# Performance work log

Hardware: AMD Instinct MI355X
Metric: run time of the kernel (lower is better)

The kernel has to match this reference:

```python
import jax, jax.numpy as jnp
import numpy as np

B, S, HID = 2, 2048, 2048
H, HD, RD, LD = 16, 128, 64, 512
AD = HD + RD  # attn_dim = 192
SCALE = 1.0 / np.sqrt(AD)


def apply_rope(x):
    """x: [B, H, S, RD] -> RoPE-rotated, matching the torch RotaryEmbedding."""
    s = x.shape[2]
    inv_freq = 1.0 / (10000.0 ** (jnp.arange(0, RD, 2, dtype=jnp.float32) / RD))
    t = jnp.arange(s, dtype=x.dtype)
    freqs = t[:, None] * inv_freq[None, :]          # [S, RD//2]
    cos, sin = jnp.cos(freqs), jnp.sin(freqs)       # broadcast over B, H
    x1, x2 = x[..., : RD // 2], x[..., RD // 2 :]
    return jnp.concatenate([x1 * cos - x2 * sin, x2 * cos + x1 * sin], axis=-1)


def setup_inputs() -> dict:
    key = jax.random.key(0)
    ks = jax.random.split(key, 7)
    std = 0.02
    return {
        "x": jax.random.normal(ks[0], (B, S, HID), jnp.float32),
        # weights stored as [in, out] (transpose of torch Linear.weight)
        "wq": jax.random.normal(ks[1], (HID, H * HD), jnp.float32) * std,
        "wq_rope": jax.random.normal(ks[2], (HID, H * RD), jnp.float32) * std,
        "wkv_down": jax.random.normal(ks[3], (HID, LD), jnp.float32) * std,
        "wkv_up": jax.random.normal(ks[4], (LD, H * 2 * HD), jnp.float32) * std,
        "wk_rope": jax.random.normal(ks[5], (HID, RD), jnp.float32) * std,
        "wo": jax.random.normal(ks[6], (H * AD, HID), jnp.float32) * std,
    }


def reference(x, wq, wq_rope, wkv_down, wkv_up, wk_rope, wo):
    b, s, _ = x.shape
    # query paths
    q_nope = (x @ wq).reshape(b, s, H, HD).transpose(0, 2, 1, 3)        # [B,H,S,HD]
    q_rope = (x @ wq_rope).reshape(b, s, H, RD).transpose(0, 2, 1, 3)   # [B,H,S,RD]
    q_rope = apply_rope(q_rope)
    q = jnp.concatenate([q_nope, q_rope], axis=-1)                      # [B,H,S,AD]
    # low-rank KV latent upcast
    kv_latent = x @ wkv_down                                            # [B,S,LD]
    kv = (kv_latent @ wkv_up).reshape(b, s, H, 2 * HD).transpose(0, 2, 1, 3)
    k_nope, v = kv[..., :HD], kv[..., HD:]                              # [B,H,S,HD]
    # shared rope key, broadcast over heads
    k_rope = jnp.broadcast_to((x @ wk_rope)[:, None], (b, H, s, RD))
    k_rope = apply_rope(k_rope)
    k = jnp.concatenate([k_nope, k_rope], axis=-1)                      # [B,H,S,AD]
    # zero-pad V to attn_dim
    v_pad = jnp.pad(v, ((0, 0), (0, 0), (0, 0), (0, RD)))
    # attention (causal)
    scores = jnp.einsum("bhqd,bhkd->bhqk", q, k) * SCALE
    causal = jnp.tril(jnp.ones((s, s), bool))
    scores = jnp.where(causal, scores, jnp.finfo(scores.dtype).min)
    probs = jax.nn.softmax(scores, axis=-1)
    attn = jnp.einsum("bhqk,bhkd->bhqd", probs, v_pad)                  # [B,H,S,AD]
    attn = attn.transpose(0, 2, 1, 3).reshape(b, s, H * AD)
    return attn @ wo
```

## Files before the change

kernel.cpp:

```cpp
#include <hip/hip_runtime.h>
#include <math.h>

#define HB 2
#define HS 2048
#define HHID 2048
#define HH 16
#define HHD 128
#define HRD 64
#define HLD 512
#define HAD 192
#define HM (HB*HS)

static __device__ __constant__ float C1_SCALE_LOG2E = 0.1041175465f;

typedef unsigned short US;
typedef __attribute__((ext_vector_type(8))) short s8v;
typedef __attribute__((ext_vector_type(4))) float f4v;
typedef __attribute__((ext_vector_type(16))) float f16v;

#if __has_builtin(__builtin_amdgcn_exp2f)
#define EXP2F __builtin_amdgcn_exp2f
#else
#define EXP2F exp2f
#endif

__device__ __forceinline__ US f2b(float f){
  union { float f; unsigned u; } v; v.f = f;
  unsigned r = v.u + 0x7fffu + ((v.u >> 16) & 1u);
  return (US)(r >> 16);
}
__device__ __forceinline__ float b2f(US u){
  union { unsigned u; float f; } v; v.u = ((unsigned)u) << 16; return v.f;
}
__device__ __forceinline__ f4v mfma16(s8v a, s8v b, f4v c){
  return __builtin_amdgcn_mfma_f32_16x16x32_bf16(a, b, c, 0, 0, 0);
}
__device__ __forceinline__ f16v mfma32(s8v a, s8v b, f16v c){
  return __builtin_amdgcn_mfma_f32_32x32x16_bf16(a, b, c, 0, 0, 0);
}
__device__ __forceinline__ void gload_lds16(const void* g, void* l){
  __builtin_amdgcn_global_load_lds((const __attribute__((address_space(1))) void*)g,
                                   (__attribute__((address_space(3))) void*)l, 16, 0, 0);
}

__global__ __launch_bounds__(256) void k_cast(const float* __restrict__ in, US* __restrict__ out, int n){
  int i = (blockIdx.x * 256 + threadIdx.x) * 4;
  if (i >= n) return;
  float4 v = *(const float4*)(in + i);
  union { US q[4]; unsigned u[2]; } p;
  p.q[0] = f2b(v.x); p.q[1] = f2b(v.y); p.q[2] = f2b(v.z); p.q[3] = f2b(v.w);
  *(uint2*)(out + i) = make_uint2(p.u[0], p.u[1]);
}

__global__ __launch_bounds__(256) void k_rope_tab(float2* __restrict__ tab){
  int idx = blockIdx.x * 256 + threadIdx.x;
  int s = idx >> 5, i = idx & 31;
  float invf = expf(-9.210340371976184f * (float)i / 32.f);
  float fr = (float)s * invf;
  tab[idx] = make_float2(cosf(fr), sinf(fr));
}

template<int WOMAP>
__global__ __launch_bounds__(256) void k_transpose_cast(const float* __restrict__ W, US* __restrict__ Wt, int K, int N){
  __shared__ float t[32][33];
  int n0 = blockIdx.x * 32, k0 = blockIdx.y * 32;
  int tx = threadIdx.x, ty = threadIdx.y;
  #pragma unroll
  for (int r = 0; r < 32; r += 8){
    int k = k0 + ty + r;
    int sk = WOMAP ? ((k >> 7) * 192 + (k & 127)) : k;
    t[ty + r][tx] = W[(size_t)sk * N + n0 + tx];
  }
  __syncthreads();
  #pragma unroll
  for (int r = 0; r < 32; r += 8){
    Wt[(size_t)(n0 + ty + r) * K + k0 + tx] = f2b(t[tx][ty + r]);
  }
}

__global__ __launch_bounds__(256) void k_transpose_v(const US* __restrict__ v, US* __restrict__ vT){
  __shared__ US t[32][33];
  int bh = blockIdx.z;
  int s0 = blockIdx.x * 32, d0 = blockIdx.y * 32;
  const US* src = v + (size_t)bh * HS * HHD;
  US* dst = vT + (size_t)bh * HHD * HS;
  int tx = threadIdx.x, ty = threadIdx.y;
  #pragma unroll
  for (int r = 0; r < 32; r += 8)
    t[ty + r][tx] = src[(size_t)(s0 + ty + r) * HHD + d0 + tx];
  __syncthreads();
  #pragma unroll
  for (int r = 0; r < 32; r += 8)
    dst[(size_t)(d0 + ty + r) * HS + s0 + tx] = t[tx][ty + r];
}

template<int EPI>
__global__ __launch_bounds__(256, 2) void k_gemm2(
    const US* __restrict__ A, const US* __restrict__ Bt,
    void* __restrict__ out0, void* __restrict__ out1, void* __restrict__ out2,
    int Kdim, int Ndim)
{
  __shared__ US As[2][128 * 64];
  __shared__ US Bs[2][128 * 64];
  const int tid = threadIdx.x;
  const int lane = tid & 63, w = tid >> 6;
  const int r15 = lane & 15, kh = lane >> 4;
  const int gx = gridDim.x;
  const int flat = blockIdx.y * gx + blockIdx.x;
  const int cpx = (gx * gridDim.y) >> 3;
  const int swz = (flat & 7) * cpx + (flat >> 3);
  const int m0 = (swz / gx) * 128, n0 = (swz % gx) * 128;
  const int wm = (w >> 1) * 64, wn = (w & 1) * 64;
  const int rsw = (r15 & 7) << 4;
  f4v acc[4][4] = {};

  auto STAGE = [&](int k0, int bb){
    #pragma unroll
    for (int j = 0; j < 4; ++j){
      int c = j * 256 + tid;
      int row = c >> 3, colD = (c & 7) * 16;
      gload_lds16((const char*)A + ((size_t)(m0 + row) * Kdim + k0) * 2 + (colD ^ ((row & 7) << 4)),
                  (char*)As[bb] + c * 16);
    }
    #pragma unroll
    for (int j = 0; j < 4; ++j){
      int c = j * 256 + tid;
      int row = c >> 3, colD = (c & 7) * 16;
      gload_lds16((const char*)Bt + ((size_t)(n0 + row) * Kdim + k0) * 2 + (colD ^ ((row & 7) << 4)),
                  (char*)Bs[bb] + c * 16);
    }
  };

  const int nk = Kdim >> 6;
  STAGE(0, 0);
  for (int t = 0; t < nk; ++t){
    if (t + 1 < nk){
      STAGE((t + 1) * 64, (t + 1) & 1);
      asm volatile("s_waitcnt vmcnt(8)" ::: "memory");
    } else {
      asm volatile("s_waitcnt vmcnt(0)" ::: "memory");
    }
    __builtin_amdgcn_s_barrier();
    __builtin_amdgcn_sched_barrier(0);
    const char* AB = (const char*)As[t & 1];
    const char* BB = (const char*)Bs[t & 1];
    #pragma unroll
    for (int ks = 0; ks < 2; ++ks){
      s8v af[4];
      #pragma unroll
      for (int mi = 0; mi < 4; ++mi)
        af[mi] = *(const s8v*)(AB + (wm + mi * 16 + r15) * 128 + ((ks * 64 + kh * 16) ^ rsw));
      #pragma unroll
      for (int ni = 0; ni < 4; ++ni){
        s8v bf = *(const s8v*)(BB + (wn + ni * 16 + r15) * 128 + ((ks * 64 + kh * 16) ^ rsw));
        #pragma unroll
        for (int mi = 0; mi < 4; ++mi)
          acc[mi][ni] = mfma16(af[mi], bf, acc[mi][ni]);
      }
    }
    __builtin_amdgcn_s_barrier();
  }

  #pragma unroll
  for (int mi = 0; mi < 4; ++mi){
    #pragma unroll
    for (int ni = 0; ni < 4; ++ni){
      #pragma unroll
      for (int j = 0; j < 4; ++j){
        float v = acc[mi][ni][j];
        int m = m0 + wm + mi * 16 + kh * 4 + j;
        int n = n0 + wn + ni * 16 + r15;
        if (EPI == 3){
          int b = m >> 11, s = m & 2047;
          int h = n >> 8, r = n & 255;
          if (r < 128)
            ((US*)out0)[((size_t)(b * HH + h) * HS + s) * HAD + r] = f2b(v);
          else
            ((US*)out1)[((size_t)(b * HH + h) * HS + s) * HHD + (r - 128)] = f2b(v);
        } else if (EPI == 4){
          ((float*)out0)[(size_t)m * HHID + n] = v;
        } else {
          int b = m >> 11, s = m & 2047;
          if (n < 2048){
            int h = n >> 7, d = n & 127;
            ((US*)out0)[((size_t)(b * HH + h) * HS + s) * HAD + d] = f2b(v);
          } else if (n < 3072){
            int dd2 = n - 2048;
            int h = dd2 >> 6, dd = dd2 & 63;
            float partner = acc[mi][ni ^ 2][j];
            float2 cs = ((const float2*)out1)[s * 32 + (dd & 31)];
            float o = (dd < 32) ? (v * cs.x - partner * cs.y) : (v * cs.x + partner * cs.y);
            ((US*)out0)[((size_t)(b * HH + h) * HS + s) * HAD + HHD + dd] = f2b(o);
          } else {
            ((US*)out2)[(size_t)m * HLD + (n - 3072)] = f2b(v);
          }
        }
      }
    }
  }
}

__global__ __launch_bounds__(256) void k_krope2(const US* __restrict__ A, const US* __restrict__ Bt,
                                                US* __restrict__ kbuf, const float2* __restrict__ tab)
{
  __shared__ US As[2][128 * 32];
  __shared__ US Bs[2][64 * 32];
  const int tid = threadIdx.x, lane = tid & 63, w = tid >> 6;
  const int r15 = lane & 15, kh = lane >> 4;
  const int m0 = blockIdx.x * 128;
  const int wm = w * 32;
  f4v acc[2][4] = {};

  auto STAGE = [&](int k0, int bb){
    #pragma unroll
    for (int j = 0; j < 2; ++j){
      int c = (w * 2 + j) * 64 + lane;
      int row = c >> 2, cc = c & 3;
      gload_lds16(A + (size_t)(m0 + row) * HHID + k0 + cc * 8, (char*)As[bb] + (w * 2 + j) * 1024);
    }
    {
      int c = w * 64 + lane;
      int row = c >> 2, cc = c & 3;
      gload_lds16(Bt + (size_t)row * HHID + k0 + cc * 8, (char*)Bs[bb] + w * 1024);
    }
  };

  STAGE(0, 0);
  for (int t = 0; t < 64; ++t){
    if (t + 1 < 64){
      STAGE((t + 1) * 32, (t + 1) & 1);
      asm volatile("s_waitcnt vmcnt(3)" ::: "memory");
    } else {
      asm volatile("s_waitcnt vmcnt(0)" ::: "memory");
    }
    __builtin_amdgcn_s_barrier();
    __builtin_amdgcn_sched_barrier(0);
    const US* AB = As[t & 1];
    const US* BB = Bs[t & 1];
    s8v af[2];
    #pragma unroll
    for (int mi = 0; mi < 2; ++mi)
      af[mi] = *(const s8v*)&AB[(wm + mi * 16 + r15) * 32 + kh * 8];
    #pragma unroll
    for (int ni = 0; ni < 4; ++ni){
      s8v bf = *(const s8v*)&BB[(ni * 16 + r15) * 32 + kh * 8];
      #pragma unroll
      for (int mi = 0; mi < 2; ++mi)
        acc[mi][ni] = mfma16(af[mi], bf, acc[mi][ni]);
    }
    __builtin_amdgcn_s_barrier();
  }

  #pragma unroll
  for (int mi = 0; mi < 2; ++mi){
    #pragma unroll
    for (int ni = 0; ni < 4; ++ni){
      #pragma unroll
      for (int j = 0; j < 4; ++j){
        float v = acc[mi][ni][j];
        float p = acc[mi][ni ^ 2][j];
        int m = m0 + wm + mi * 16 + kh * 4 + j;
        int b = m >> 11, s = m & 2047;
        int n = ni * 16 + r15;
        float2 cs = tab[s * 32 + (n & 31)];
        float o = (n < 32) ? (v * cs.x - p * cs.y) : (v * cs.x + p * cs.y);
        US ob = f2b(o);
        US* base = kbuf + ((size_t)(b * HH) * HS + s) * HAD + HHD + n;
        #pragma unroll
        for (int h = 0; h < 16; ++h)
          base[(size_t)h * HS * HAD] = ob;
      }
    }
  }
}

__global__ __launch_bounds__(256, 2) void k_attn(
    const US* __restrict__ qbuf, const US* __restrict__ kbuf,
    const US* __restrict__ vT, US* __restrict__ attnb)
{
  __shared__ US Ks[2][64 * 192];
  __shared__ US Vs[2][128 * 64];

  const int tid = threadIdx.x, lane = tid & 63, w = tid >> 6;
  const int l31 = lane & 31, hi = lane >> 5;
  const int bid = blockIdx.x;
  const int bh = bid & 31, b = bh >> 4, head = bh & 15;
  const int u = (bid < 256) ? (15 - (bid >> 5)) : ((bid - 256) >> 5);
  const int q0 = u * 128;
  const int qw0 = q0 + w * 32;
  const int qrow = qw0 + l31;
  const int sw = (l31 & 7) << 4;

  const char* qb = (const char*)(qbuf + (size_t)bh * HS * HAD);
  const char* kb = (const char*)(kbuf + (size_t)bh * HS * HAD);
  const char* vb = (const char*)(vT   + (size_t)bh * HHD * HS);

  s8v qf[12];
  {
    const char* qr = qb + (size_t)qrow * 384;
    #pragma unroll
    for (int ks = 0; ks < 12; ++ks)
      qf[ks] = *(const s8v*)(qr + ks * 32 + hi * 16);
  }

  auto STAGE = [&](int tt, int bb){
    const int k0s = tt * 64;
    #pragma unroll
    for (int j = 0; j < 6; ++j){
      int c = j * 256 + tid;
      int row = c / 24, colD = (c - row * 24) * 16;
      gload_lds16(kb + (size_t)(k0s + row) * 384 + (colD ^ ((row & 7) << 4)),
                  (char*)Ks[bb] + (j * 4 + w) * 1024);
    }
    #pragma unroll
    for (int j = 0; j < 4; ++j){
      int c = j * 256 + tid;
      int d = c >> 3, colD = (c & 7) * 16;
      gload_lds16(vb + (size_t)d * (HS * 2) + (size_t)k0s * 2 + (colD ^ ((d & 7) << 4)),
                  (char*)Vs[bb] + (j * 4 + w) * 1024);
    }
  };

  f16v acc_o[4] = {};
  float mraw = -3e38f, lsum = 0.f;

  const int nt = (q0 + 128) >> 6;
  STAGE(0, 0);
  for (int t = 0; t < nt; ++t){
    if (t + 1 < nt){
      STAGE(t + 1, (t + 1) & 1);
      asm volatile("s_waitcnt vmcnt(10)" ::: "memory");
    } else {
      asm volatile("s_waitcnt vmcnt(0)" ::: "memory");
    }
    __builtin_amdgcn_s_barrier();
    __builtin_amdgcn_sched_barrier(0);

    const int k0 = t * 64;
    if (k0 <= qw0 + 31){
      const char* KB = (const char*)Ks[t & 1];
      const char* VB = (const char*)Vs[t & 1];
      f16v sacc[2] = {};
      #pragma unroll
      for (int ks = 0; ks < 12; ++ks){
        #pragma unroll
        for (int ni = 0; ni < 2; ++ni){
          s8v kf = *(const s8v*)(KB + (ni * 32 + l31) * 384 + ((ks * 32 + hi * 16) ^ sw));
          sacc[ni] = mfma32(kf, qf[ks], sacc[ni]);
        }
      }

      const bool need_mask = (k0 + 63 > qrow);
      float mx = -3e38f;
      #pragma unroll
      for (int ni = 0; ni < 2; ++ni){
        #pragma unroll
        for (int r = 0; r < 16; ++r){
          float s = sacc[ni][r];
          if (need_mask){
            int kv = k0 + ni * 32 + (r & 3) + 8 * (r >> 2) + 4 * hi;
            if (kv > qrow) s = -3e38f;
            sacc[ni][r] = s;
          }
          mx = fmaxf(mx, s);
        }
      }
      mx = fmaxf(mx, __shfl_xor(mx, 32));

      float scl = 1.0f;
      if (__any(mx > mraw + 76.8f)){
        float mnew = fmaxf(mraw, mx);
        scl = EXP2F((mraw - mnew) * C1_SCALE_LOG2E);
        mraw = mnew;
        #pragma unroll
        for (int r = 0; r < 16; ++r){
          float sb = __shfl(scl, (r & 3) + 8 * (r >> 2) + 4 * hi);
          #pragma unroll
          for (int db = 0; db < 4; ++db)
            acc_o[db][r] *= sb;
        }
      }

      float m2 = mraw * C1_SCALE_LOG2E;
      float rs = 0.f;
      #pragma unroll
      for (int ni = 0; ni < 2; ++ni){
        #pragma unroll
        for (int r = 0; r < 16; ++r){
          float p = EXP2F(fmaf(sacc[ni][r], C1_SCALE_LOG2E, -m2));
          sacc[ni][r] = p;
          rs += p;
        }
      }
      rs += __shfl_xor(rs, 32);
      lsum = lsum * scl + rs;

      union PU { s8v v; unsigned u[4]; } pa[4];
      #pragma unroll
      for (int ni = 0; ni < 2; ++ni){
        #pragma unroll
        for (int g = 0; g < 2; ++g){
          unsigned a0, a1, b0, b1;
          const int rb = g * 8;
          asm("v_cvt_pk_bf16_f32 %0, %1, %2" : "=v"(a0) : "v"(sacc[ni][rb + 0]), "v"(sacc[ni][rb + 1]));
          asm("v_cvt_pk_bf16_f32 %0, %1, %2" : "=v"(a1) : "v"(sacc[ni][rb + 2]), "v"(sacc[ni][rb + 3]));
          asm("v_cvt_pk_bf16_f32 %0, %1, %2" : "=v"(b0) : "v"(sacc[ni][rb + 4]), "v"(sacc[ni][rb + 5]));
          asm("v_cvt_pk_bf16_f32 %0, %1, %2" : "=v"(b1) : "v"(sacc[ni][rb + 6]), "v"(sacc[ni][rb + 7]));
          asm("v_permlane32_swap_b32 %0, %1" : "+v"(a0), "+v"(b0));
          asm("v_permlane32_swap_b32 %0, %1" : "+v"(a1), "+v"(b1));
          pa[ni * 2 + g].u[0] = a0; pa[ni * 2 + g].u[1] = a1;
          pa[ni * 2 + g].u[2] = b0; pa[ni * 2 + g].u[3] = b1;
        }
      }

      #pragma unroll
      for (int ks2 = 0; ks2 < 4; ++ks2){
        #pragma unroll
        for (int db = 0; db < 4; ++db){
          s8v vf = *(const s8v*)(VB + (db * 32 + l31) * 128 + ((ks2 * 32 + hi * 16) ^ sw));
          acc_o[db] = mfma32(pa[ks2].v, vf, acc_o[db]);
        }
      }
    }
    __builtin_amdgcn_s_barrier();
  }

  float linv = 1.0f / lsum;
  #pragma unroll
  for (int r = 0; r < 16; ++r){
    int crow = (r & 3) + 8 * (r >> 2) + 4 * hi;
    float lb = __shfl(linv, crow);
    int qq = qw0 + crow;
    US* dst = attnb + (size_t)(b * HS + qq) * (HH * HHD) + head * HHD;
    #pragma unroll
    for (int db = 0; db < 4; ++db)
      dst[db * 32 + l31] = f2b(acc_o[db][r] * lb);
  }
}

extern "C" void kernel_launch(void* const* d_in, const int* in_sizes, int n_in,
                              void* d_out, int out_size, void* d_ws, size_t ws_size,
                              hipStream_t stream)
{
  (void)in_sizes; (void)n_in; (void)out_size; (void)ws_size;
  const float* x        = (const float*)d_in[0];
  const float* wq       = (const float*)d_in[1];
  const float* wq_rope  = (const float*)d_in[2];
  const float* wkv_down = (const float*)d_in[3];
  const float* wkv_up   = (const float*)d_in[4];
  const float* wk_rope  = (const float*)d_in[5];
  const float* wo       = (const float*)d_in[6];

  char* ws = (char*)d_ws;
  size_t off = 0;
  auto alloc = [&](size_t bytes)->void*{ void* p = ws + off; off += (bytes + 255) & ~(size_t)255; return p; };

  US* xb     = (US*)alloc((size_t)HM * HHID * 2);
  US* wqT    = (US*)alloc((size_t)2048 * 2048 * 2);
  US* wqrT   = (US*)alloc((size_t)1024 * 2048 * 2);
  US* wkvdT  = (US*)alloc((size_t)512 * 2048 * 2);
  US* wkvuT  = (US*)alloc((size_t)4096 * 512 * 2);
  US* wkrT   = (US*)alloc((size_t)64 * 2048 * 2);
  US* woT    = (US*)alloc((size_t)2048 * 2048 * 2);
  US* qbuf   = (US*)alloc((size_t)32 * HS * HAD * 2);
  US* kbuf   = (US*)alloc((size_t)32 * HS * HAD * 2);
  US* vbuf   = (US*)alloc((size_t)32 * HS * HHD * 2);
  US* vTb    = (US*)alloc((size_t)32 * HS * HHD * 2);
  US* latent = (US*)alloc((size_t)HM * HLD * 2);
  float2* tab = (float2*)alloc((size_t)HS * 32 * 8);
  US* attnb = xb;

  dim3 tb(256);
  dim3 t328(32, 8);

  k_cast<<<dim3(8192), tb, 0, stream>>>(x, xb, HM * HHID);
  k_rope_tab<<<dim3(256), tb, 0, stream>>>(tab);
  k_transpose_cast<0><<<dim3(64, 64),  t328, 0, stream>>>(wq,       wqT,   2048, 2048);
  k_transpose_cast<0><<<dim3(32, 64),  t328, 0, stream>>>(wq_rope,  wqrT,  2048, 1024);
  k_transpose_cast<0><<<dim3(16, 64),  t328, 0, stream>>>(wkv_down, wkvdT, 2048, 512);
  k_transpose_cast<0><<<dim3(128, 16), t328, 0, stream>>>(wkv_up,   wkvuT, 512,  4096);
  k_transpose_cast<0><<<dim3(2, 64),   t328, 0, stream>>>(wk_rope,  wkrT,  2048, 64);
  k_transpose_cast<1><<<dim3(64, 64),  t328, 0, stream>>>(wo,       woT,   2048, 2048);

  k_gemm2<5><<<dim3(28, 32), tb, 0, stream>>>(xb, wqT, (void*)qbuf, (void*)tab, (void*)latent, 2048, 3584);
  k_gemm2<3><<<dim3(32, 32), tb, 0, stream>>>(latent, wkvuT, (void*)kbuf, (void*)vbuf, (void*)nullptr, 512, 4096);
  k_krope2<<<dim3(32), tb, 0, stream>>>(xb, wkrT, kbuf, tab);
  k_transpose_v<<<dim3(64, 4, 32), t328, 0, stream>>>(vbuf, vTb);
  k_attn<<<dim3(512), tb, 0, stream>>>(qbuf, kbuf, vTb, attnb);
  k_gemm2<4><<<dim3(16, 32), tb, 0, stream>>>(attnb, woT, d_out, (void*)nullptr, (void*)nullptr, 2048, 2048);
}
```

Before: 308.0 us.

## Fuse k-rope projection into QKV GEMM and enlarge GEMM tiles to 256x128

The shared rope-key projection is folded into the first projection GEMM. Its transposed weight is placed contiguously after the other weights, and a zero-padded block rounds N up to a multiple of 128. A new epilogue branch applies RoPE and broadcasts the result to all 16 heads in kbuf, which removes the separate, poorly parallel k_krope2 launch. All GEMMs also move to 512-thread blocks with a 256-row M tile, so each B tile is reused across more rows. The cost is half as many blocks, one block per CU, and an extra memset for the padding.

```diff
diff --git a/kernel.cpp b/kernel.cpp
--- a/kernel.cpp
+++ b/kernel.cpp
@@ -95,12 +95,13 @@
 }
 
 template<int EPI>
-__global__ __launch_bounds__(256, 2) void k_gemm2(
+__global__ __launch_bounds__(512, 1) void k_gemm2(
     const US* __restrict__ A, const US* __restrict__ Bt,
-    void* __restrict__ out0, void* __restrict__ out1, void* __restrict__ out2,
+    void* __restrict__ out0, void* __restrict__ out1,
+    void* __restrict__ out2, void* __restrict__ out3,
     int Kdim, int Ndim)
 {
-  __shared__ US As[2][128 * 64];
+  __shared__ US As[2][256 * 64];
   __shared__ US Bs[2][128 * 64];
   const int tid = threadIdx.x;
   const int lane = tid & 63, w = tid >> 6;
@@ -109,7 +110,7 @@
   const int flat = blockIdx.y * gx + blockIdx.x;
   const int cpx = (gx * gridDim.y) >> 3;
   const int swz = (flat & 7) * cpx + (flat >> 3);
-  const int m0 = (swz / gx) * 128, n0 = (swz % gx) * 128;
+  const int m0 = (swz / gx) * 256, n0 = (swz % gx) * 128;
   const int wm = (w >> 1) * 64, wn = (w & 1) * 64;
   const int rsw = (r15 & 7) << 4;
   f4v acc[4][4] = {};
@@ -117,14 +118,14 @@
   auto STAGE = [&](int k0, int bb){
     #pragma unroll
     for (int j = 0; j < 4; ++j){
-      int c = j * 256 + tid;
+      int c = j * 512 + tid;
       int row = c >> 3, colD = (c & 7) * 16;
       gload_lds16((const char*)A + ((size_t)(m0 + row) * Kdim + k0) * 2 + (colD ^ ((row & 7) << 4)),
                   (char*)As[bb] + c * 16);
     }
     #pragma unroll
-    for (int j = 0; j < 4; ++j){
-      int c = j * 256 + tid;
+    for (int j = 0; j < 2; ++j){
+      int c = j * 512 + tid;
       int row = c >> 3, colD = (c & 7) * 16;
       gload_lds16((const char*)Bt + ((size_t)(n0 + row) * Kdim + k0) * 2 + (colD ^ ((row & 7) << 4)),
                   (char*)Bs[bb] + c * 16);
@@ -136,7 +137,7 @@
   for (int t = 0; t < nk; ++t){
     if (t + 1 < nk){
       STAGE((t + 1) * 64, (t + 1) & 1);
-      asm volatile("s_waitcnt vmcnt(8)" ::: "memory");
+      asm volatile("s_waitcnt vmcnt(6)" ::: "memory");
     } else {
       asm volatile("s_waitcnt vmcnt(0)" ::: "memory");
     }
@@ -191,84 +192,20 @@
             float2 cs = ((const float2*)out1)[s * 32 + (dd & 31)];
             float o = (dd < 32) ? (v * cs.x - partner * cs.y) : (v * cs.x + partner * cs.y);
             ((US*)out0)[((size_t)(b * HH + h) * HS + s) * HAD + HHD + dd] = f2b(o);
-          } else {
+          } else if (n < 3584){
             ((US*)out2)[(size_t)m * HLD + (n - 3072)] = f2b(v);
+          } else if (n < 3648){
+            int dd = n - 3584;
+            float partner = acc[mi][ni ^ 2][j];
+            float2 cs = ((const float2*)out1)[s * 32 + (dd & 31)];
+            float o = (dd < 32) ? (v * cs.x - partner * cs.y) : (v * cs.x + partner * cs.y);
+            US ob = f2b(o);
+            US* base = (US*)out3 + ((size_t)(b * HH) * HS + s) * HAD + HHD + dd;
+            #pragma unroll
+            for (int h = 0; h < 16; ++h)
+              base[(size_t)h * HS * HAD] = ob;
           }
         }
-      }
-    }
-  }
-}
-
-__global__ __launch_bounds__(256) void k_krope2(const US* __restrict__ A, const US* __restrict__ Bt,
-                                                US* __restrict__ kbuf, const float2* __restrict__ tab)
-{
-  __shared__ US As[2][128 * 32];
-  __shared__ US Bs[2][64 * 32];
-  const int tid = threadIdx.x, lane = tid & 63, w = tid >> 6;
-  const int r15 = lane & 15, kh = lane >> 4;
-  const int m0 = blockIdx.x * 128;
-  const int wm = w * 32;
-  f4v acc[2][4] = {};
-
-  auto STAGE = [&](int k0, int bb){
-    #pragma unroll
-    for (int j = 0; j < 2; ++j){
-      int c = (w * 2 + j) * 64 + lane;
-      int row = c >> 2, cc = c & 3;
-      gload_lds16(A + (size_t)(m0 + row) * HHID + k0 + cc * 8, (char*)As[bb] + (w * 2 + j) * 1024);
-    }
-    {
-      int c = w * 64 + lane;
-      int row = c >> 2, cc = c & 3;
-      gload_lds16(Bt + (size_t)row * HHID + k0 + cc * 8, (char*)Bs[bb] + w * 1024);
-    }
-  };
-
-  STAGE(0, 0);
-  for (int t = 0; t < 64; ++t){
-    if (t + 1 < 64){
-      STAGE((t + 1) * 32, (t + 1) & 1);
-      asm volatile("s_waitcnt vmcnt(3)" ::: "memory");
-    } else {
-      asm volatile("s_waitcnt vmcnt(0)" ::: "memory");
-    }
-    __builtin_amdgcn_s_barrier();
-    __builtin_amdgcn_sched_barrier(0);
-    const US* AB = As[t & 1];
-    const US* BB = Bs[t & 1];
-    s8v af[2];
-    #pragma unroll
-    for (int mi = 0; mi < 2; ++mi)
-      af[mi] = *(const s8v*)&AB[(wm + mi * 16 + r15) * 32 + kh * 8];
-    #pragma unroll
-    for (int ni = 0; ni < 4; ++ni){
-      s8v bf = *(const s8v*)&BB[(ni * 16 + r15) * 32 + kh * 8];
-      #pragma unroll
-      for (int mi = 0; mi < 2; ++mi)
-        acc[mi][ni] = mfma16(af[mi], bf, acc[mi][ni]);
-    }
-    __builtin_amdgcn_s_barrier();
-  }
-
-  #pragma unroll
-  for (int mi = 0; mi < 2; ++mi){
-    #pragma unroll
-    for (int ni = 0; ni < 4; ++ni){
-      #pragma unroll
-      for (int j = 0; j < 4; ++j){
-        float v = acc[mi][ni][j];
-        float p = acc[mi][ni ^ 2][j];
-        int m = m0 + wm + mi * 16 + kh * 4 + j;
-        int b = m >> 11, s = m & 2047;
-        int n = ni * 16 + r15;
-        float2 cs = tab[s * 32 + (n & 31)];
-        float o = (n < 32) ? (v * cs.x - p * cs.y) : (v * cs.x + p * cs.y);
-        US ob = f2b(o);
-        US* base = kbuf + ((size_t)(b * HH) * HS + s) * HAD + HHD + n;
-        #pragma unroll
-        for (int h = 0; h < 16; ++h)
-          base[(size_t)h * HS * HAD] = ob;
       }
     }
   }
@@ -459,8 +396,9 @@
   US* wqT    = (US*)alloc((size_t)2048 * 2048 * 2);
   US* wqrT   = (US*)alloc((size_t)1024 * 2048 * 2);
   US* wkvdT  = (US*)alloc((size_t)512 * 2048 * 2);
+  US* wkrT   = (US*)alloc((size_t)64 * 2048 * 2);
+  US* wkrPad = (US*)alloc((size_t)64 * 2048 * 2);
   US* wkvuT  = (US*)alloc((size_t)4096 * 512 * 2);
-  US* wkrT   = (US*)alloc((size_t)64 * 2048 * 2);
   US* woT    = (US*)alloc((size_t)2048 * 2048 * 2);
   US* qbuf   = (US*)alloc((size_t)32 * HS * HAD * 2);
   US* kbuf   = (US*)alloc((size_t)32 * HS * HAD * 2);
@@ -473,6 +411,7 @@
   dim3 tb(256);
   dim3 t328(32, 8);
 
+  hipMemsetAsync(wkrPad, 0, (size_t)64 * 2048 * 2, stream);
   k_cast<<<dim3(8192), tb, 0, stream>>>(x, xb, HM * HHID);
   k_rope_tab<<<dim3(256), tb, 0, stream>>>(tab);
   k_transpose_cast<0><<<dim3(64, 64),  t328, 0, stream>>>(wq,       wqT,   2048, 2048);
@@ -482,10 +421,9 @@
   k_transpose_cast<0><<<dim3(2, 64),   t328, 0, stream>>>(wk_rope,  wkrT,  2048, 64);
   k_transpose_cast<1><<<dim3(64, 64),  t328, 0, stream>>>(wo,       woT,   2048, 2048);
 
-  k_gemm2<5><<<dim3(28, 32), tb, 0, stream>>>(xb, wqT, (void*)qbuf, (void*)tab, (void*)latent, 2048, 3584);
-  k_gemm2<3><<<dim3(32, 32), tb, 0, stream>>>(latent, wkvuT, (void*)kbuf, (void*)vbuf, (void*)nullptr, 512, 4096);
-  k_krope2<<<dim3(32), tb, 0, stream>>>(xb, wkrT, kbuf, tab);
+  k_gemm2<5><<<dim3(29, 16), dim3(512), 0, stream>>>(xb, wqT, (void*)qbuf, (void*)tab, (void*)latent, (void*)kbuf, 2048, 3712);
+  k_gemm2<3><<<dim3(32, 16), dim3(512), 0, stream>>>(latent, wkvuT, (void*)kbuf, (void*)vbuf, (void*)nullptr, (void*)nullptr, 512, 4096);
   k_transpose_v<<<dim3(64, 4, 32), t328, 0, stream>>>(vbuf, vTb);
   k_attn<<<dim3(512), tb, 0, stream>>>(qbuf, kbuf, vTb, attnb);
-  k_gemm2<4><<<dim3(16, 32), tb, 0, stream>>>(attnb, woT, d_out, (void*)nullptr, (void*)nullptr, 2048, 2048);
-}
+  k_gemm2<4><<<dim3(16, 16), dim3(512), 0, stream>>>(attnb, woT, d_out, (void*)nullptr, (void*)nullptr, (void*)nullptr, 2048, 2048);
+}
```

Measured after the change: 323.8 us. +5.1%, slower.
